# Performance work log

Measured on AMD Instinct MI355X. Metric: run time of the kernel, lower is better.

The kernel has to match this reference:

```python
import jax, jax.numpy as jnp
import numpy as np

B, N, C, H, CLS = 16, 1024, 768, 12, 1000
M = 0.5  # amax init for alpha


def setup_inputs() -> dict:
    key = jax.random.key(0)
    k = jax.random.split(key, 7)
    x = jax.random.normal(k[0], (B, N, C), jnp.float32)
    label = jax.random.randint(k[1], (B,), 0, CLS)
    # alpha is initialized to ones*m in the module; add small noise so gating is non-trivial
    alpha = jnp.ones((CLS, 3 * C), jnp.float32) * M + 0.1 * jax.random.normal(k[2], (CLS, 3 * C), jnp.float32)
    qkv_w = jax.random.normal(k[3], (3 * C, C), jnp.float32) * 0.02
    qkv_b = jax.random.normal(k[4], (3 * C,), jnp.float32) * 0.02
    proj_w = jax.random.normal(k[5], (C, C), jnp.float32) * 0.02
    proj_b = jax.random.normal(k[6], (C,), jnp.float32) * 0.02
    return {"x": x, "label": label, "alpha": alpha, "qkv_w": qkv_w,
            "qkv_b": qkv_b, "proj_w": proj_w, "proj_b": proj_b}


def reference(x, label, alpha, qkv_w, qkv_b, proj_w, proj_b):
    b, n, c = x.shape
    h = H
    hd = c // h
    scale = hd ** -0.5
    # per-sample sigmoid gate over the 3C output rows of the qkv projection
    sig = jax.nn.sigmoid(alpha[label])  # (B, 3C)
    # F.linear(x_i, W * s_i[:,None], b * s_i) == (x_i @ W.T) * s_i + b * s_i
    qkv = jnp.einsum('bnc,dc->bnd', x, qkv_w) * sig[:, None, :] + (qkv_b * sig)[:, None, :]
    qkv = qkv.reshape(b, n, 3, h, hd).transpose(2, 0, 3, 1, 4)  # (3, B, H, N, hd)
    q, k_, v = qkv[0], qkv[1], qkv[2]
    attn = jax.nn.softmax(jnp.einsum('bhqd,bhkd->bhqk', q, k_) * scale, axis=-1)
    out = jnp.einsum('bhqk,bhkd->bhqd', attn, v)          # (B, H, N, hd)
    out = out.transpose(0, 2, 1, 3).reshape(b, n, c)       # (B, N, C)
    out = out @ proj_w.T + proj_b
    return out
```

## Files before the change

### kernel.cpp

```cpp
#include <hip/hip_runtime.h>

typedef __bf16 bf16;
typedef __attribute__((ext_vector_type(8))) __bf16 bf16x8;
typedef __attribute__((ext_vector_type(4))) float floatx4;
typedef __attribute__((ext_vector_type(8))) short short8;
typedef __attribute__((ext_vector_type(4))) short short4v;
typedef unsigned short u16;

#define B_  16
#define N_  1024
#define C_  768
#define H_  12
#define HD_ 64
#define TC_ 2304
#define QSZ (B_ * H_ * N_ * HD_)

__device__ __forceinline__ u16 f2b(float f) { bf16 h = (bf16)f; return __builtin_bit_cast(u16, h); }

typedef __attribute__((address_space(1))) const unsigned int guint;
typedef __attribute__((address_space(3))) unsigned int luint;
__device__ __forceinline__ void gl16(const u16* g, u16* l) {
    __builtin_amdgcn_global_load_lds((guint*)g, (luint*)l, 16, 0, 0);
}

__global__ __launch_bounds__(256) void cvt_swz(
    const float* __restrict__ x, const float* __restrict__ qw,
    const float* __restrict__ pw, u16* __restrict__ xb,
    u16* __restrict__ qwb, u16* __restrict__ pwb)
{
    const int gid = blockIdx.x * 256 + threadIdx.x;
    const int b   = gid & 7;
    const int rb  = gid >> 3;
    const int row = rb / 12, g = rb - row * 12;
    const float* src; u16* dst; int r;
    if (row < 16384)      { src = x;  dst = xb;  r = row; }
    else if (row < 18688) { src = qw; dst = qwb; r = row - 16384; }
    else                  { src = pw; dst = pwb; r = row - 18688; }
    const float* sp = src + (size_t)r * 768 + g * 64 + b * 8;
    floatx4 a = *(const floatx4*)sp;
    floatx4 c = *(const floatx4*)(sp + 4);
    short8 v;
    v[0] = (short)f2b(a[0]); v[1] = (short)f2b(a[1]);
    v[2] = (short)f2b(a[2]); v[3] = (short)f2b(a[3]);
    v[4] = (short)f2b(c[0]); v[5] = (short)f2b(c[1]);
    v[6] = (short)f2b(c[2]); v[7] = (short)f2b(c[3]);
    *(short8*)(dst + (size_t)r * 768 + g * 64 + (b ^ (r & 7)) * 8) = v;
}

template <int MODE>
__global__ __launch_bounds__(256, 4) void gemm_bt(
    const u16* __restrict__ A, const u16* __restrict__ W,
    const float* __restrict__ bias, const float* __restrict__ alpha,
    const int* __restrict__ label, void* __restrict__ out, u16* __restrict__ vT)
{
    __shared__ __align__(16) u16 sm[16384];
    u16* sA = sm;
    u16* sB = sm + 8192;
    const int t  = threadIdx.x;
    const int w  = t >> 6, l = t & 63;
    const int lr = l & 15, lq = l >> 4;
    const int id = blockIdx.x;
    const int xcd = id & 7, j = id >> 3;
    const int m0 = (xcd * 16 + (j & 15)) << 7;
    const int n0 = (j >> 4) << 7;
    const int wm = (w >> 1) << 6, wn = (w & 1) << 6;
    const int sw = lr & 7;

    floatx4 acc[4][4];
#pragma unroll
    for (int a = 0; a < 4; a++)
#pragma unroll
        for (int b = 0; b < 4; b++) acc[a][b] = (floatx4){0.f, 0.f, 0.f, 0.f};

    const int cx8  = (t & 7) * 8;
    const int row0 = t >> 3;

    auto a_off = [&](int r, int ks) -> int {
        const int m = m0 + r;
        if (MODE == 0) return m * 768 + ks * 64 + cx8;
        return (((m >> 10) * H_ + ks) * N_ + (m & (N_ - 1))) * HD_ + cx8;
    };

    const int nk = 12;
    for (int ks = 0; ks < nk; ++ks) {
        __syncthreads();
#pragma unroll
        for (int i = 0; i < 4; i++) {
            gl16(A + a_off(row0 + 32 * i, ks), sA + i * 2048 + t * 8);
            gl16(W + (n0 + row0 + 32 * i) * 768 + ks * 64 + cx8, sB + i * 2048 + t * 8);
        }
        __syncthreads();
#pragma unroll
        for (int kc = 0; kc < 2; kc++) {
            bf16x8 af[4], bfr[4];
#pragma unroll
            for (int mt = 0; mt < 4; mt++)
                af[mt] = *(const bf16x8*)(sA + (wm + mt * 16 + lr) * 64 + 8 * ((kc * 4 + lq) ^ sw));
#pragma unroll
            for (int nt = 0; nt < 4; nt++)
                bfr[nt] = *(const bf16x8*)(sB + (wn + nt * 16 + lr) * 64 + 8 * ((kc * 4 + lq) ^ sw));
#pragma unroll
            for (int mt = 0; mt < 4; mt++)
#pragma unroll
                for (int nt = 0; nt < 4; nt++)
                    acc[mt][nt] = __builtin_amdgcn_mfma_f32_16x16x32_bf16(af[mt], bfr[nt], acc[mt][nt], 0, 0, 0);
        }
    }

    if (MODE == 0) {
        const int b   = m0 >> 10;
        const int lab = label[b];
        const int which = (n0 >= 1536) ? 2 : (n0 >= 768 ? 1 : 0);
        if (which == 2) {
#pragma unroll
            for (int nt = 0; nt < 4; nt++) {
                const int d3   = n0 + wn + nt * 16 + lr;
                const float sg = 1.f / (1.f + __expf(-alpha[lab * TC_ + d3]));
                const float bv = bias[d3];
                const int rcol = d3 - 1536;
                const int h = rcol >> 6, dd = rcol & 63;
                u16* vp = vT + (((b * H_ + h) * HD_ + dd) << 10);
#pragma unroll
                for (int mt = 0; mt < 4; mt++) {
                    const int nb = (m0 & 1023) + wm + mt * 16 + lq * 4;
                    const int sidx = (nb & ~63) + 8 * (((nb >> 3) & 7) ^ (dd & 7)) + (nb & 7);
                    short4v pk;
#pragma unroll
                    for (int i = 0; i < 4; i++) pk[i] = (short)f2b((acc[mt][nt][i] + bv) * sg);
                    *(short4v*)(vp + sidx) = pk;
                }
            }
        } else {
            float sgv[4], bvv[4];
#pragma unroll
            for (int nt = 0; nt < 4; nt++) {
                const int d3 = n0 + wn + nt * 16 + lr;
                sgv[nt] = 1.f / (1.f + __expf(-alpha[lab * TC_ + d3]));
                bvv[nt] = bias[d3];
            }
            const int hbase = (n0 - which * 768) >> 6;
            const int nb0   = m0 & 1023;
            u16* ob = (u16*)out + which * QSZ;
#pragma unroll
            for (int p = 0; p < 2; p++) {
                __syncthreads();
                if (wm == p * 64) {
#pragma unroll
                    for (int nt = 0; nt < 4; nt++) {
                        const int c = wn + nt * 16 + lr;
#pragma unroll
                        for (int mt = 0; mt < 4; mt++)
#pragma unroll
                            for (int i = 0; i < 4; i++)
                                sm[(mt * 16 + lq * 4 + i) * 132 + c] =
                                    f2b((acc[mt][nt][i] + bvv[nt]) * sgv[nt]);
                    }
                }
                __syncthreads();
#pragma unroll
                for (int hh = 0; hh < 2; hh++) {
                    u16* dsth = ob + ((((b * H_ + hbase + hh) << 10) + nb0 + p * 64) << 6);
#pragma unroll
                    for (int mi = 0; mi < 2; mi++) {
                        const int m = (t >> 3) + 32 * mi;
                        *(short8*)(dsth + m * 64 + (t & 7) * 8) =
                            *(const short8*)(sm + m * 132 + hh * 64 + 8 * ((t & 7) ^ (m & 7)));
                    }
                }
            }
        }
    } else {
        float bvv[4];
#pragma unroll
        for (int nt = 0; nt < 4; nt++) bvv[nt] = bias[n0 + wn + nt * 16 + lr];
        __syncthreads();
        float* swf = (float*)sm + w * (16 * 68);
        const int rr = l >> 2, c0 = (l & 3) * 16;
#pragma unroll
        for (int mt = 0; mt < 4; mt++) {
#pragma unroll
            for (int nt = 0; nt < 4; nt++)
#pragma unroll
                for (int i = 0; i < 4; i++)
                    swf[(lq * 4 + i) * 68 + nt * 16 + lr] = acc[mt][nt][i] + bvv[nt];
            float* drow = (float*)out + (m0 + wm + mt * 16 + rr) * 768 + n0 + wn + c0;
#pragma unroll
            for (int jj = 0; jj < 4; jj++)
                *(floatx4*)(drow + jj * 4) = *(const floatx4*)(swf + rr * 68 + c0 + jj * 4);
        }
    }
}

__global__ __launch_bounds__(256, 4) void attn_fwd(
    u16* __restrict__ qb, const u16* __restrict__ kb, const u16* __restrict__ vtb)
{
    __shared__ __align__(16) u16 sQP[64 * 64];
    __shared__ __align__(16) u16 sK[2][64 * 64];
    __shared__ __align__(16) u16 sVt[2][64 * 64];

    const int t = threadIdx.x, w = t >> 6, l = t & 63;
    const int lr = l & 15, lq = l >> 4;
    const int id = blockIdx.x;
    const int r8 = id & 7, s = id >> 3;
    const int bh = r8 * 24 + (s >> 4);
    const int q0 = (s & 15) << 6;
    const int sw = lr & 7;

    const u16* kgb = kb + bh * (N_ * HD_);
    const u16* vgb = vtb + bh * (HD_ * N_);
    const int vrow = t >> 3, vcol = (t & 7) * 8;

    auto stage = [&](int kt, int bufi) {
        const u16* gk = kgb + kt * 4096;
        gl16(gk + t * 8,        sK[bufi] + t * 8);
        gl16(gk + 2048 + t * 8, sK[bufi] + 2048 + t * 8);
        const u16* gv = vgb + kt * 64;
        gl16(gv + vrow * N_ + vcol,        sVt[bufi] + t * 8);
        gl16(gv + (vrow + 32) * N_ + vcol, sVt[bufi] + 2048 + t * 8);
    };

    u16* qg = qb + (bh * N_ + q0) * HD_;
    gl16(qg + t * 8,        sQP + t * 8);
    gl16(qg + 2048 + t * 8, sQP + 2048 + t * 8);
    stage(0, 0);
    __syncthreads();

    bf16x8 qf[2];
#pragma unroll
    for (int kc = 0; kc < 2; kc++)
        qf[kc] = *(const bf16x8*)(sQP + (w * 16 + lr) * 64 + 8 * ((kc * 4 + lq) ^ sw));

    float l_run = 0.f;
    floatx4 o_acc[4];
#pragma unroll
    for (int nt = 0; nt < 4; nt++) o_acc[nt] = (floatx4){0.f, 0.f, 0.f, 0.f};

#pragma unroll 2
    for (int kt = 0; kt < 16; ++kt) {
        const int cb = kt & 1;
        if (kt < 15) stage(kt + 1, cb ^ 1);

        floatx4 st[4];
#pragma unroll
        for (int mt = 0; mt < 4; mt++) st[mt] = (floatx4){0.f, 0.f, 0.f, 0.f};
        __builtin_amdgcn_s_setprio(1);
#pragma unroll
        for (int kc = 0; kc < 2; kc++) {
#pragma unroll
            for (int mt = 0; mt < 4; mt++) {
                bf16x8 kf = *(const bf16x8*)(sK[cb] + (mt * 16 + lr) * 64 + 8 * ((kc * 4 + lq) ^ sw));
                st[mt] = __builtin_amdgcn_mfma_f32_16x16x32_bf16(kf, qf[kc], st[mt], 0, 0, 0);
            }
        }
        __builtin_amdgcn_s_setprio(0);

        float rs0 = 0.f, rs1 = 0.f;
        u16 pb[4][4];
#pragma unroll
        for (int mt = 0; mt < 4; mt++) {
#pragma unroll
            for (int i = 0; i < 4; i++) {
                const float p = __builtin_amdgcn_exp2f(
                    fmaf(st[mt][i], 0.18033688011112f, -11.54156032711171f));
                pb[mt][i] = f2b(p);
                if (mt & 1) rs1 += p; else rs0 += p;
            }
        }
        float rs = rs0 + rs1;
        rs += __shfl_xor(rs, 16, 64);
        rs += __shfl_xor(rs, 32, 64);
        l_run += rs;
#pragma unroll
        for (int mt = 0; mt < 4; mt++) {
            short4v pk;
#pragma unroll
            for (int i = 0; i < 4; i++) pk[i] = (short)pb[mt][i];
            *(short4v*)(sQP + (w * 16 + lr) * 64 +
                        8 * ((mt * 2 + (lq >> 1)) ^ sw) + (lq & 1) * 4) = pk;
        }
        __builtin_amdgcn_s_setprio(1);
#pragma unroll
        for (int kc = 0; kc < 2; kc++) {
            bf16x8 pf = *(const bf16x8*)(sQP + (w * 16 + lr) * 64 + 8 * ((kc * 4 + lq) ^ sw));
#pragma unroll
            for (int nt = 0; nt < 4; nt++) {
                bf16x8 vf = *(const bf16x8*)(sVt[cb] + (nt * 16 + lr) * 64 + 8 * ((kc * 4 + lq) ^ sw));
                o_acc[nt] = __builtin_amdgcn_mfma_f32_16x16x32_bf16(pf, vf, o_acc[nt], 0, 0, 0);
            }
        }
        __builtin_amdgcn_s_setprio(0);
        __syncthreads();
    }

    const float linv = 1.f / l_run;
#pragma unroll
    for (int nt = 0; nt < 4; nt++) {
#pragma unroll
        for (int i = 0; i < 4; i++) {
            const float lv = __shfl(linv, lq * 4 + i, 64);
            const int row = w * 16 + lq * 4 + i;
            sQP[row * 64 + 8 * ((nt * 2 + (lr >> 3)) ^ (row & 7)) + (lr & 7)] = f2b(o_acc[nt][i] * lv);
        }
    }
    __syncthreads();
#pragma unroll
    for (int i2 = 0; i2 < 2; i2++) {
        const int idx = i2 * 2048 + t * 8;
        *(short8*)(qg + idx) = *(const short8*)(sQP + idx);
    }
}

extern "C" void kernel_launch(void* const* d_in, const int* in_sizes, int n_in,
                              void* d_out, int out_size, void* d_ws, size_t ws_size,
                              hipStream_t stream)
{
    const float* x      = (const float*)d_in[0];
    const int*   label  = (const int*)d_in[1];
    const float* alpha  = (const float*)d_in[2];
    const float* qkv_w  = (const float*)d_in[3];
    const float* qkv_b  = (const float*)d_in[4];
    const float* proj_w = (const float*)d_in[5];
    const float* proj_b = (const float*)d_in[6];

    u16* xb    = (u16*)d_ws;
    u16* qwb   = xb + (size_t)16384 * 768;
    u16* pwb   = qwb + (size_t)2304 * 768;
    u16* qbuf  = pwb + (size_t)768 * 768;
    u16* kbuf  = qbuf + QSZ;
    u16* vtbuf = kbuf + QSZ;

    cvt_swz<<<7296, 256, 0, stream>>>(x, qkv_w, proj_w, xb, qwb, pwb);
    gemm_bt<0><<<2304, 256, 0, stream>>>(xb, qwb, qkv_b, alpha, label, qbuf, vtbuf);
    attn_fwd<<<3072, 256, 0, stream>>>(qbuf, kbuf, vtbuf);
    gemm_bt<1><<<768, 256, 0, stream>>>(qbuf, pwb, proj_b, nullptr, nullptr, d_out, nullptr);
}
```

Before: 313.6 us.

## Replace 128x128 GEMM with 256x256 double-buffered async-load GEMM

Result: no change. 308.0 us (-1.8%).

```diff
diff --git a/kernel.cpp b/kernel.cpp
--- a/kernel.cpp
+++ b/kernel.cpp
@@ -48,145 +48,170 @@
 }
 
 template <int MODE>
-__global__ __launch_bounds__(256, 4) void gemm_bt(
+__global__ __launch_bounds__(512, 2) void gemm256(
     const u16* __restrict__ A, const u16* __restrict__ W,
     const float* __restrict__ bias, const float* __restrict__ alpha,
     const int* __restrict__ label, void* __restrict__ out, u16* __restrict__ vT)
 {
-    __shared__ __align__(16) u16 sm[16384];
-    u16* sA = sm;
-    u16* sB = sm + 8192;
+    __shared__ __align__(16) u16 sm[65536];
     const int t  = threadIdx.x;
     const int w  = t >> 6, l = t & 63;
-    const int lr = l & 15, lq = l >> 4;
+    const int lr = l & 15, lq = l >> 4, sw = lr & 7;
+    const int wr = w >> 2, wc = w & 3;
     const int id = blockIdx.x;
-    const int xcd = id & 7, j = id >> 3;
-    const int m0 = (xcd * 16 + (j & 15)) << 7;
-    const int n0 = (j >> 4) << 7;
-    const int wm = (w >> 1) << 6, wn = (w & 1) << 6;
-    const int sw = lr & 7;
-
-    floatx4 acc[4][4];
-#pragma unroll
-    for (int a = 0; a < 4; a++)
+    const int xcd = id & 7, jj = id >> 3;
+    const int n_t = jj >> 3;
+    const int m_t = xcd * 8 + (jj & 7);
+    const int m0 = m_t << 8, n0 = n_t << 8;
+
+    floatx4 acc[8][4];
+#pragma unroll
+    for (int a = 0; a < 8; a++)
 #pragma unroll
         for (int b = 0; b < 4; b++) acc[a][b] = (floatx4){0.f, 0.f, 0.f, 0.f};
 
-    const int cx8  = (t & 7) * 8;
-    const int row0 = t >> 3;
-
-    auto a_off = [&](int r, int ks) -> int {
+    const int cx8 = (t & 7) * 8;
+    const int r0  = t >> 3;
+
+    auto a_gaddr = [&](int r, int kt) -> const u16* {
         const int m = m0 + r;
-        if (MODE == 0) return m * 768 + ks * 64 + cx8;
-        return (((m >> 10) * H_ + ks) * N_ + (m & (N_ - 1))) * HD_ + cx8;
-    };
-
-    const int nk = 12;
-    for (int ks = 0; ks < nk; ++ks) {
-        __syncthreads();
-#pragma unroll
-        for (int i = 0; i < 4; i++) {
-            gl16(A + a_off(row0 + 32 * i, ks), sA + i * 2048 + t * 8);
-            gl16(W + (n0 + row0 + 32 * i) * 768 + ks * 64 + cx8, sB + i * 2048 + t * 8);
-        }
-        __syncthreads();
-#pragma unroll
-        for (int kc = 0; kc < 2; kc++) {
-            bf16x8 af[4], bfr[4];
-#pragma unroll
-            for (int mt = 0; mt < 4; mt++)
-                af[mt] = *(const bf16x8*)(sA + (wm + mt * 16 + lr) * 64 + 8 * ((kc * 4 + lq) ^ sw));
-#pragma unroll
-            for (int nt = 0; nt < 4; nt++)
-                bfr[nt] = *(const bf16x8*)(sB + (wn + nt * 16 + lr) * 64 + 8 * ((kc * 4 + lq) ^ sw));
-#pragma unroll
-            for (int mt = 0; mt < 4; mt++)
+        if (MODE == 0) return A + m * 768 + kt * 64 + cx8;
+        return A + (size_t)((((m >> 10) * H_ + kt) << 10) + (m & 1023)) * HD_ + cx8;
+    };
+    auto stage = [&](int kt, int b) {
+#pragma unroll
+        for (int h = 0; h < 2; h++)
+#pragma unroll
+            for (int p = 0; p < 2; p++) {
+                gl16(a_gaddr(h * 128 + p * 64 + r0, kt),
+                     sm + (b * 2 + h) * 8192 + p * 4096 + t * 8);
+                gl16(W + (n0 + h * 128 + p * 64 + r0) * 768 + kt * 64 + cx8,
+                     sm + 32768 + (b * 2 + h) * 8192 + p * 4096 + t * 8);
+            }
+    };
+    auto tile = [&](int b) {
+        bf16x8 bfrg[4][2];
+#pragma unroll
+        for (int nt = 0; nt < 4; nt++)
+#pragma unroll
+            for (int kc = 0; kc < 2; kc++)
+                bfrg[nt][kc] = *(const bf16x8*)(sm + 32768 + (b * 2 + (wc >> 1)) * 8192 +
+                                ((wc & 1) * 64 + nt * 16 + lr) * 64 + 8 * ((kc * 4 + lq) ^ sw));
+#pragma unroll
+        for (int mh = 0; mh < 2; mh++) {
+            bf16x8 afrg[4][2];
+#pragma unroll
+            for (int mi = 0; mi < 4; mi++)
+#pragma unroll
+                for (int kc = 0; kc < 2; kc++)
+                    afrg[mi][kc] = *(const bf16x8*)(sm + (b * 2 + wr) * 8192 +
+                                    ((mh * 4 + mi) * 16 + lr) * 64 + 8 * ((kc * 4 + lq) ^ sw));
+            __builtin_amdgcn_s_setprio(1);
+#pragma unroll
+            for (int mi = 0; mi < 4; mi++)
 #pragma unroll
                 for (int nt = 0; nt < 4; nt++)
-                    acc[mt][nt] = __builtin_amdgcn_mfma_f32_16x16x32_bf16(af[mt], bfr[nt], acc[mt][nt], 0, 0, 0);
-        }
-    }
+#pragma unroll
+                    for (int kc = 0; kc < 2; kc++)
+                        acc[mh * 4 + mi][nt] = __builtin_amdgcn_mfma_f32_16x16x32_bf16(
+                            afrg[mi][kc], bfrg[nt][kc], acc[mh * 4 + mi][nt], 0, 0, 0);
+            __builtin_amdgcn_s_setprio(0);
+        }
+    };
+    auto tile_step = [&](int b, bool last) {
+        if (last) asm volatile("s_waitcnt vmcnt(0)" ::: "memory");
+        else      asm volatile("s_waitcnt vmcnt(8)" ::: "memory");
+        __builtin_amdgcn_sched_barrier(0);
+        __builtin_amdgcn_s_barrier();
+        __builtin_amdgcn_sched_barrier(0);
+        tile(b);
+        asm volatile("" ::: "memory");
+        __builtin_amdgcn_s_barrier();
+        __builtin_amdgcn_sched_barrier(0);
+    };
+
+    stage(0, 0);
+    stage(1, 1);
+#pragma unroll 1
+    for (int i = 0; i < 5; ++i) {
+        tile_step(0, false); stage(2 * i + 2, 0);
+        tile_step(1, false); stage(2 * i + 3, 1);
+    }
+    tile_step(0, false);
+    tile_step(1, true);
 
     if (MODE == 0) {
-        const int b   = m0 >> 10;
-        const int lab = label[b];
+        const int bI  = m0 >> 10;
+        const int lab = label[bI];
         const int which = (n0 >= 1536) ? 2 : (n0 >= 768 ? 1 : 0);
+        const int pos0 = (m0 & 1023) + wr * 128;
+        const int h = (n0 + wc * 64 - which * 768) >> 6;
+        u16* ws = sm + w * 8192;
+        float sg[4], bv[4];
+#pragma unroll
+        for (int nt = 0; nt < 4; nt++) {
+            const int d3 = n0 + wc * 64 + nt * 16 + lr;
+            sg[nt] = 1.f / (1.f + __expf(-alpha[lab * TC_ + d3]));
+            bv[nt] = bias[d3];
+        }
         if (which == 2) {
 #pragma unroll
             for (int nt = 0; nt < 4; nt++) {
-                const int d3   = n0 + wn + nt * 16 + lr;
-                const float sg = 1.f / (1.f + __expf(-alpha[lab * TC_ + d3]));
-                const float bv = bias[d3];
-                const int rcol = d3 - 1536;
-                const int h = rcol >> 6, dd = rcol & 63;
-                u16* vp = vT + (((b * H_ + h) * HD_ + dd) << 10);
-#pragma unroll
-                for (int mt = 0; mt < 4; mt++) {
-                    const int nb = (m0 & 1023) + wm + mt * 16 + lq * 4;
-                    const int sidx = (nb & ~63) + 8 * (((nb >> 3) & 7) ^ (dd & 7)) + (nb & 7);
-                    short4v pk;
-#pragma unroll
-                    for (int i = 0; i < 4; i++) pk[i] = (short)f2b((acc[mt][nt][i] + bv) * sg);
-                    *(short4v*)(vp + sidx) = pk;
-                }
+                const int dd = nt * 16 + lr;
+#pragma unroll
+                for (int mt = 0; mt < 8; mt++)
+#pragma unroll
+                    for (int i = 0; i < 4; i++) {
+                        const int p = mt * 16 + lq * 4 + i;
+                        ws[dd * 128 + (p & 64) + 8 * (((p >> 3) & 7) ^ (dd & 7)) + (p & 7)]
+                            = f2b((acc[mt][nt][i] + bv[nt]) * sg[nt]);
+                    }
+            }
+#pragma unroll
+            for (int it = 0; it < 16; ++it) {
+                const int dd = it * 4 + (l >> 4);
+                const int ch = l & 15;
+                *(short8*)(vT + ((((size_t)(bI * H_ + h) << 6) + dd) << 10) + pos0 + ch * 8)
+                    = *(const short8*)(ws + dd * 128 + ch * 8);
             }
         } else {
-            float sgv[4], bvv[4];
-#pragma unroll
-            for (int nt = 0; nt < 4; nt++) {
-                const int d3 = n0 + wn + nt * 16 + lr;
-                sgv[nt] = 1.f / (1.f + __expf(-alpha[lab * TC_ + d3]));
-                bvv[nt] = bias[d3];
-            }
-            const int hbase = (n0 - which * 768) >> 6;
-            const int nb0   = m0 & 1023;
-            u16* ob = (u16*)out + which * QSZ;
-#pragma unroll
-            for (int p = 0; p < 2; p++) {
-                __syncthreads();
-                if (wm == p * 64) {
-#pragma unroll
-                    for (int nt = 0; nt < 4; nt++) {
-                        const int c = wn + nt * 16 + lr;
-#pragma unroll
-                        for (int mt = 0; mt < 4; mt++)
-#pragma unroll
-                            for (int i = 0; i < 4; i++)
-                                sm[(mt * 16 + lq * 4 + i) * 132 + c] =
-                                    f2b((acc[mt][nt][i] + bvv[nt]) * sgv[nt]);
+#pragma unroll
+            for (int mt = 0; mt < 8; mt++)
+#pragma unroll
+                for (int nt = 0; nt < 4; nt++)
+#pragma unroll
+                    for (int i = 0; i < 4; i++) {
+                        const int p = mt * 16 + lq * 4 + i;
+                        const int d = nt * 16 + lr;
+                        ws[p * 64 + 8 * ((d >> 3) ^ (p & 7)) + (d & 7)]
+                            = f2b((acc[mt][nt][i] + bv[nt]) * sg[nt]);
                     }
-                }
-                __syncthreads();
-#pragma unroll
-                for (int hh = 0; hh < 2; hh++) {
-                    u16* dsth = ob + ((((b * H_ + hbase + hh) << 10) + nb0 + p * 64) << 6);
-#pragma unroll
-                    for (int mi = 0; mi < 2; mi++) {
-                        const int m = (t >> 3) + 32 * mi;
-                        *(short8*)(dsth + m * 64 + (t & 7) * 8) =
-                            *(const short8*)(sm + m * 132 + hh * 64 + 8 * ((t & 7) ^ (m & 7)));
-                    }
-                }
+            u16* ob = (u16*)out + which * QSZ + ((((bI * H_ + h) << 10) + pos0) << 6);
+#pragma unroll
+            for (int it = 0; it < 16; ++it) {
+                const int p = it * 8 + (l >> 3);
+                const int ch = l & 7;
+                *(short8*)(ob + p * 64 + ch * 8) = *(const short8*)(ws + p * 64 + ch * 8);
             }
         }
     } else {
-        float bvv[4];
-#pragma unroll
-        for (int nt = 0; nt < 4; nt++) bvv[nt] = bias[n0 + wn + nt * 16 + lr];
-        __syncthreads();
+        float bv[4];
+#pragma unroll
+        for (int nt = 0; nt < 4; nt++) bv[nt] = bias[n0 + wc * 64 + nt * 16 + lr];
         float* swf = (float*)sm + w * (16 * 68);
         const int rr = l >> 2, c0 = (l & 3) * 16;
 #pragma unroll
-        for (int mt = 0; mt < 4; mt++) {
+        for (int mt = 0; mt < 8; mt++) {
 #pragma unroll
             for (int nt = 0; nt < 4; nt++)
 #pragma unroll
                 for (int i = 0; i < 4; i++)
-                    swf[(lq * 4 + i) * 68 + nt * 16 + lr] = acc[mt][nt][i] + bvv[nt];
-            float* drow = (float*)out + (m0 + wm + mt * 16 + rr) * 768 + n0 + wn + c0;
-#pragma unroll
-            for (int jj = 0; jj < 4; jj++)
-                *(floatx4*)(drow + jj * 4) = *(const floatx4*)(swf + rr * 68 + c0 + jj * 4);
+                    swf[(lq * 4 + i) * 68 + nt * 16 + lr] = acc[mt][nt][i] + bv[nt];
+            float* drow = (float*)out + (size_t)(m0 + wr * 128 + mt * 16 + rr) * 768
+                          + n0 + wc * 64 + c0;
+#pragma unroll
+            for (int jf = 0; jf < 4; jf++)
+                *(floatx4*)(drow + jf * 4) = *(const floatx4*)(swf + rr * 68 + c0 + jf * 4);
         }
     }
 }
@@ -330,7 +355,7 @@
     u16* vtbuf = kbuf + QSZ;
 
     cvt_swz<<<7296, 256, 0, stream>>>(x, qkv_w, proj_w, xb, qwb, pwb);
-    gemm_bt<0><<<2304, 256, 0, stream>>>(xb, qwb, qkv_b, alpha, label, qbuf, vtbuf);
+    gemm256<0><<<576, 512, 0, stream>>>(xb, qwb, qkv_b, alpha, label, qbuf, vtbuf);
     attn_fwd<<<3072, 256, 0, stream>>>(qbuf, kbuf, vtbuf);
-    gemm_bt<1><<<768, 256, 0, stream>>>(qbuf, pwb, proj_b, nullptr, nullptr, d_out, nullptr);
-}
+    gemm256<1><<<192, 512, 0, stream>>>(qbuf, pwb, proj_b, nullptr, nullptr, d_out, nullptr);
+}
```
